# Kernel optimization log

Hardware: AMD Instinct MI355X
Metric: run time of the kernel (lower is better)

The kernel has to match this reference:

```python
import jax, jax.numpy as jnp
import numpy as np

B, S, H, F, E = 2, 2048, 1024, 4096, 8  # batch, seq, hidden, ffn, num_experts


def setup_inputs() -> dict:
    key = jax.random.key(0)
    ks = jax.random.split(key, 4)
    x = jax.random.normal(ks[0], (B, S, H), dtype=jnp.float32)
    w_router = jax.random.normal(ks[1], (H, E), dtype=jnp.float32) * 0.02
    w1 = jax.random.normal(ks[2], (E, H, F), dtype=jnp.float32) * 0.02
    b1 = jnp.zeros((E, F), dtype=jnp.float32)
    w2 = jax.random.normal(ks[3], (E, F, H), dtype=jnp.float32) * 0.02
    b2 = jnp.zeros((E, H), dtype=jnp.float32)
    return {"x": x, "w_router": w_router, "w1": w1, "b1": b1, "w2": w2, "b2": b2}


def reference(x, w_router, w1, b1, w2, b2):
    """Top-1 MoE layer: route -> per-expert FFN -> weighted combine.

    Faithful to ExpertParallelWrapper._process_moe_layer on a single group:
    router picks one expert per token with a routing weight; tokens are
    dispatched to experts (here expressed as a static mask over the fixed
    expert set), processed by the expert FFN, and scatter-combined back
    weighted by the routing probability.
    """
    Bs, Ss, Hs = x.shape
    n_experts = w1.shape[0]
    # Router: per-token logits -> softmax -> top-1 expert + weight
    logits = jnp.einsum('bsh,he->bse', x, w_router)          # [B,S,E]
    probs = jax.nn.softmax(logits, axis=-1)
    sel = jnp.argmax(probs, axis=-1)                          # [B,S] selected expert
    wgt = jnp.take_along_axis(probs, sel[..., None], axis=-1)[..., 0]  # [B,S]

    xt = x.reshape(-1, Hs)        # [T,H] flat tokens
    sel_t = sel.reshape(-1)       # [T]
    wgt_t = wgt.reshape(-1)       # [T]

    out = jnp.zeros_like(xt)
    # Static loop over the small fixed expert set (dispatch/combine via mask).
    for e in range(n_experts):
        h = jax.nn.relu(xt @ w1[e] + b1[e])   # [T,F]
        y = h @ w2[e] + b2[e]                 # [T,H]
        m = (sel_t == e).astype(xt.dtype) * wgt_t
        out = out + m[:, None] * y
    return out.reshape(Bs, Ss, Hs)
```

## Files before the change

kernel.cpp:

```cpp
#include <hip/hip_runtime.h>
#include <math.h>

#define T_TOK 4096
#define H_DIM 1024
#define F_DIM 4096
#define E_NUM 8
#define BK 32

typedef __attribute__((ext_vector_type(8))) short bhalf8_t;
typedef __attribute__((ext_vector_type(4))) float f32x4_t;

__device__ __forceinline__ unsigned short f2bf(float f) {
  unsigned int u = __float_as_uint(f);
  return (unsigned short)((u + 0x7fffu + ((u >> 16) & 1u)) >> 16);
}

__device__ __forceinline__ void gload16(const void* g, void* l) {
  __builtin_amdgcn_global_load_lds(
      (const __attribute__((address_space(1))) unsigned int*)g,
      (__attribute__((address_space(3))) unsigned int*)l, 16, 0, 0);
}

__global__ void k_init(int* counts) {
  if (threadIdx.x < E_NUM) counts[threadIdx.x] = 0;
}

__global__ void k_router(const float* __restrict__ x, const float* __restrict__ wr,
                         int* __restrict__ sel, float* __restrict__ wgt,
                         int* __restrict__ counts) {
  const int t = blockIdx.x;
  const int lane = threadIdx.x;
  const float* xr = x + (size_t)t * H_DIM;
  double acc[E_NUM] = {0, 0, 0, 0, 0, 0, 0, 0};
  for (int h = lane; h < H_DIM; h += 64) {
    const double xv = (double)xr[h];
    const float* w = wr + (size_t)h * E_NUM;
#pragma unroll
    for (int e = 0; e < E_NUM; ++e) acc[e] += xv * (double)w[e];
  }
#pragma unroll
  for (int e = 0; e < E_NUM; ++e) {
#pragma unroll
    for (int off = 32; off > 0; off >>= 1) acc[e] += __shfl_down(acc[e], off, 64);
  }
  if (lane == 0) {
    double m = acc[0];
    int a = 0;
#pragma unroll
    for (int e = 1; e < E_NUM; ++e)
      if (acc[e] > m) { m = acc[e]; a = e; }
    double s = 0.0;
#pragma unroll
    for (int e = 0; e < E_NUM; ++e) s += exp(acc[e] - m);
    sel[t] = a;
    wgt[t] = (float)(1.0 / s);
    atomicAdd(&counts[a], 1);
  }
}

__global__ void k_prefix(const int* __restrict__ counts, int* __restrict__ offs,
                         int* __restrict__ cursors) {
  if (threadIdx.x == 0 && blockIdx.x == 0) {
    int s = 0;
    for (int e = 0; e < E_NUM; ++e) {
      offs[e] = s;
      cursors[e] = s;
      s += counts[e];
    }
    offs[E_NUM] = s;
  }
}

__global__ void k_scatter(const float* __restrict__ x, const int* __restrict__ sel,
                          const float* __restrict__ wgt, int* __restrict__ cursors,
                          int* __restrict__ s2t, float* __restrict__ wgtS,
                          unsigned short* __restrict__ Xs) {
  const int t = blockIdx.x;
  __shared__ int sslot;
  if (threadIdx.x == 0) {
    const int slot = atomicAdd(&cursors[sel[t]], 1);
    sslot = slot;
    s2t[slot] = t;
    wgtS[slot] = wgt[t];
  }
  __syncthreads();
  const int slot = sslot;
  const float4 v = reinterpret_cast<const float4*>(x + (size_t)t * H_DIM)[threadIdx.x];
  ushort4 o;
  o.x = f2bf(v.x); o.y = f2bf(v.y); o.z = f2bf(v.z); o.w = f2bf(v.w);
  reinterpret_cast<ushort4*>(Xs + (size_t)slot * H_DIM)[threadIdx.x] = o;
}

__global__ void k_transpose(const float* __restrict__ in, unsigned short* __restrict__ out,
                            int K, int N) {
  const int e = blockIdx.z;
  const int n0 = blockIdx.x * 64;
  const int k0 = blockIdx.y * 64;
  __shared__ float tile[64][65];
  const float* src = in + (size_t)e * K * N;
  unsigned short* dst = out + (size_t)e * N * K;
  const int tx = threadIdx.x & 63;
  const int ty = threadIdx.x >> 6;
#pragma unroll
  for (int i = 0; i < 64; i += 4)
    tile[ty + i][tx] = src[(size_t)(k0 + ty + i) * N + (n0 + tx)];
  __syncthreads();
#pragma unroll
  for (int i = 0; i < 64; i += 4)
    dst[(size_t)(n0 + ty + i) * K + (k0 + tx)] = f2bf(tile[tx][ty + i]);
}

__global__ __launch_bounds__(256) void k_ffn1(const unsigned short* __restrict__ Xs,
                                              const unsigned short* __restrict__ Wt,
                                              const float* __restrict__ b1,
                                              unsigned short* __restrict__ Hws,
                                              const int* __restrict__ offs) {
  const int e = blockIdx.z;
  const int off = offs[e];
  const int cnt = offs[e + 1] - off;
  const int m0 = blockIdx.y * 128;
  if (m0 >= cnt) return;
  const int n0 = blockIdx.x * 128;
  const int msize = cnt - m0;

  __shared__ short lA[128 * BK];
  __shared__ short lB[128 * BK];

  const int tid = threadIdx.x;
  const int lane = tid & 63;
  const int wv = tid >> 6;
  const int wm = (wv >> 1) * 64;
  const int wn = (wv & 1) * 64;

  const int sRow = lane >> 2;
  const int sCol = (lane & 3) * 8;

  const unsigned short* Abase = Xs + (size_t)off * H_DIM;
  const unsigned short* Bbase = Wt + (size_t)e * F_DIM * H_DIM + (size_t)n0 * H_DIM;

  f32x4_t acc[4][4];
#pragma unroll
  for (int i = 0; i < 4; ++i)
#pragma unroll
    for (int j = 0; j < 4; ++j) acc[i][j] = (f32x4_t){0.f, 0.f, 0.f, 0.f};

  for (int k0 = 0; k0 < H_DIM; k0 += BK) {
    __syncthreads();
#pragma unroll
    for (int i = 0; i < 2; ++i) {
      const int g = wv * 2 + i;
      const int row = g * 16 + sRow;
      int ar = row;
      if (ar >= msize) ar = 0;
      gload16(Abase + (size_t)(m0 + ar) * H_DIM + k0 + sCol, &lA[g * 16 * BK]);
      gload16(Bbase + (size_t)row * H_DIM + k0 + sCol, &lB[g * 16 * BK]);
    }
    __syncthreads();

    const int q = lane >> 4;
    const int r16 = lane & 15;
    bhalf8_t af[4], bf[4];
#pragma unroll
    for (int mi = 0; mi < 4; ++mi)
      af[mi] = *reinterpret_cast<const bhalf8_t*>(&lA[(wm + mi * 16 + r16) * BK + q * 8]);
#pragma unroll
    for (int ni = 0; ni < 4; ++ni)
      bf[ni] = *reinterpret_cast<const bhalf8_t*>(&lB[(wn + ni * 16 + r16) * BK + q * 8]);
#pragma unroll
    for (int mi = 0; mi < 4; ++mi)
#pragma unroll
      for (int ni = 0; ni < 4; ++ni)
        acc[mi][ni] = __builtin_amdgcn_mfma_f32_16x16x32_bf16(af[mi], bf[ni], acc[mi][ni], 0, 0, 0);
  }

  const int q = lane >> 4;
  const int c = lane & 15;
#pragma unroll
  for (int ni = 0; ni < 4; ++ni) {
    const int col = n0 + wn + ni * 16 + c;
    const float bias = b1[e * F_DIM + col];
#pragma unroll
    for (int mi = 0; mi < 4; ++mi) {
      const int rbase = wm + mi * 16 + q * 4;
#pragma unroll
      for (int r = 0; r < 4; ++r) {
        const int row = rbase + r;
        if (row < msize) {
          float v = acc[mi][ni][r] + bias;
          v = fmaxf(v, 0.0f);
          Hws[(size_t)(off + m0 + row) * F_DIM + col] = f2bf(v);
        }
      }
    }
  }
}

__global__ __launch_bounds__(256) void k_ffn2(const unsigned short* __restrict__ Hws,
                                              const unsigned short* __restrict__ Wt,
                                              const float* __restrict__ b2,
                                              const int* __restrict__ offs,
                                              const int* __restrict__ s2t,
                                              const float* __restrict__ wgtS,
                                              float* __restrict__ out) {
  const int e = blockIdx.z;
  const int off = offs[e];
  const int cnt = offs[e + 1] - off;
  const int m0 = blockIdx.y * 128;
  if (m0 >= cnt) return;
  const int n0 = blockIdx.x * 128;
  const int msize = cnt - m0;

  __shared__ short lA[128 * BK];
  __shared__ short lB[128 * BK];

  const int tid = threadIdx.x;
  const int lane = tid & 63;
  const int wv = tid >> 6;
  const int wm = (wv >> 1) * 64;
  const int wn = (wv & 1) * 64;

  const int sRow = lane >> 2;
  const int sCol = (lane & 3) * 8;

  const unsigned short* Abase = Hws + (size_t)off * F_DIM;
  const unsigned short* Bbase = Wt + (size_t)e * H_DIM * F_DIM + (size_t)n0 * F_DIM;

  f32x4_t acc[4][4];
#pragma unroll
  for (int i = 0; i < 4; ++i)
#pragma unroll
    for (int j = 0; j < 4; ++j) acc[i][j] = (f32x4_t){0.f, 0.f, 0.f, 0.f};

  for (int k0 = 0; k0 < F_DIM; k0 += BK) {
    __syncthreads();
#pragma unroll
    for (int i = 0; i < 2; ++i) {
      const int g = wv * 2 + i;
      const int row = g * 16 + sRow;
      int ar = row;
      if (ar >= msize) ar = 0;
      gload16(Abase + (size_t)(m0 + ar) * F_DIM + k0 + sCol, &lA[g * 16 * BK]);
      gload16(Bbase + (size_t)row * F_DIM + k0 + sCol, &lB[g * 16 * BK]);
    }
    __syncthreads();

    const int q = lane >> 4;
    const int r16 = lane & 15;
    bhalf8_t af[4], bf[4];
#pragma unroll
    for (int mi = 0; mi < 4; ++mi)
      af[mi] = *reinterpret_cast<const bhalf8_t*>(&lA[(wm + mi * 16 + r16) * BK + q * 8]);
#pragma unroll
    for (int ni = 0; ni < 4; ++ni)
      bf[ni] = *reinterpret_cast<const bhalf8_t*>(&lB[(wn + ni * 16 + r16) * BK + q * 8]);
#pragma unroll
    for (int mi = 0; mi < 4; ++mi)
#pragma unroll
      for (int ni = 0; ni < 4; ++ni)
        acc[mi][ni] = __builtin_amdgcn_mfma_f32_16x16x32_bf16(af[mi], bf[ni], acc[mi][ni], 0, 0, 0);
  }

  const int q = lane >> 4;
  const int c = lane & 15;
#pragma unroll
  for (int mi = 0; mi < 4; ++mi) {
    const int rbase = wm + mi * 16 + q * 4;
#pragma unroll
    for (int r = 0; r < 4; ++r) {
      const int row = rbase + r;
      if (row >= msize) continue;
      const int srow = off + m0 + row;
      const int tok = s2t[srow];
      const float w = wgtS[srow];
      float* orow = out + (size_t)tok * H_DIM;
#pragma unroll
      for (int ni = 0; ni < 4; ++ni) {
        const int col = n0 + wn + ni * 16 + c;
        orow[col] = w * (acc[mi][ni][r] + b2[e * H_DIM + col]);
      }
    }
  }
}

extern "C" void kernel_launch(void* const* d_in, const int* in_sizes, int n_in,
                              void* d_out, int out_size, void* d_ws, size_t ws_size,
                              hipStream_t stream) {
  const float* x  = (const float*)d_in[0];
  const float* wr = (const float*)d_in[1];
  const float* w1 = (const float*)d_in[2];
  const float* b1 = (const float*)d_in[3];
  const float* w2 = (const float*)d_in[4];
  const float* b2 = (const float*)d_in[5];
  float* out = (float*)d_out;

  char* ws = (char*)d_ws;
  unsigned short* WT  = (unsigned short*)(ws);
  unsigned short* XS  = (unsigned short*)(ws + 67108864);
  unsigned short* HWS = (unsigned short*)(ws + 67108864 + 8388608);
  char* ctrl = ws + 67108864 + 8388608 + 33554432;
  int*   sel     = (int*)(ctrl);
  int*   s2t     = (int*)(ctrl + 16384);
  float* wgt     = (float*)(ctrl + 32768);
  float* wgtS    = (float*)(ctrl + 49152);
  int*   counts  = (int*)(ctrl + 65536);
  int*   offs    = (int*)(ctrl + 65536 + 64);
  int*   cursors = (int*)(ctrl + 65536 + 128);

  k_init<<<1, 64, 0, stream>>>(counts);
  k_router<<<T_TOK, 64, 0, stream>>>(x, wr, sel, wgt, counts);
  k_prefix<<<1, 1, 0, stream>>>(counts, offs, cursors);
  k_scatter<<<T_TOK, 256, 0, stream>>>(x, sel, wgt, cursors, s2t, wgtS, XS);

  k_transpose<<<dim3(F_DIM / 64, H_DIM / 64, E_NUM), 256, 0, stream>>>(w1, WT, H_DIM, F_DIM);
  k_ffn1<<<dim3(F_DIM / 128, T_TOK / 128, E_NUM), 256, 0, stream>>>(XS, WT, b1, HWS, offs);

  k_transpose<<<dim3(H_DIM / 64, F_DIM / 64, E_NUM), 256, 0, stream>>>(w2, WT, F_DIM, H_DIM);
  k_ffn2<<<dim3(H_DIM / 128, T_TOK / 128, E_NUM), 256, 0, stream>>>(HWS, WT, b2, offs, s2t, wgtS, out);
}
```

Measured before the change: 581.4 us.

## Double GEMM K-tile, XOR-swizzle LDS, vectorize transpose, pack router blocks

The expert GEMM K-tile grows from 32 to 64, halving the number of barrier-separated load/compute iterations, and the LDS layout gets an XOR swizzle on both the global-to-LDS loads and the fragment reads to avoid bank conflicts. The weight transpose kernel now uses float4 loads and 16-byte packed bf16 stores instead of scalar accesses. The router packs four tokens per 256-thread block, and the GEMMs get a launch-bounds occupancy hint. Costs are doubled LDS per block and possible register pressure from the hint.

```diff
diff --git a/kernel.cpp b/kernel.cpp
--- a/kernel.cpp
+++ b/kernel.cpp
@@ -5,9 +5,10 @@
 #define H_DIM 1024
 #define F_DIM 4096
 #define E_NUM 8
-#define BK 32
+#define BK 64
 
 typedef __attribute__((ext_vector_type(8))) short bhalf8_t;
+typedef __attribute__((ext_vector_type(8))) unsigned short ushort8_t;
 typedef __attribute__((ext_vector_type(4))) float f32x4_t;
 
 __device__ __forceinline__ unsigned short f2bf(float f) {
@@ -25,11 +26,12 @@
   if (threadIdx.x < E_NUM) counts[threadIdx.x] = 0;
 }
 
-__global__ void k_router(const float* __restrict__ x, const float* __restrict__ wr,
-                         int* __restrict__ sel, float* __restrict__ wgt,
-                         int* __restrict__ counts) {
-  const int t = blockIdx.x;
-  const int lane = threadIdx.x;
+__global__ __launch_bounds__(256) void k_router(const float* __restrict__ x,
+                                                const float* __restrict__ wr,
+                                                int* __restrict__ sel, float* __restrict__ wgt,
+                                                int* __restrict__ counts) {
+  const int t = blockIdx.x * 4 + (threadIdx.x >> 6);
+  const int lane = threadIdx.x & 63;
   const float* xr = x + (size_t)t * H_DIM;
   double acc[E_NUM] = {0, 0, 0, 0, 0, 0, 0, 0};
   for (int h = lane; h < H_DIM; h += 64) {
@@ -91,30 +93,44 @@
   reinterpret_cast<ushort4*>(Xs + (size_t)slot * H_DIM)[threadIdx.x] = o;
 }
 
-__global__ void k_transpose(const float* __restrict__ in, unsigned short* __restrict__ out,
-                            int K, int N) {
+__global__ __launch_bounds__(256) void k_transpose(const float* __restrict__ in,
+                                                   unsigned short* __restrict__ out,
+                                                   int K, int N) {
   const int e = blockIdx.z;
   const int n0 = blockIdx.x * 64;
   const int k0 = blockIdx.y * 64;
   __shared__ float tile[64][65];
   const float* src = in + (size_t)e * K * N;
   unsigned short* dst = out + (size_t)e * N * K;
-  const int tx = threadIdx.x & 63;
-  const int ty = threadIdx.x >> 6;
-#pragma unroll
-  for (int i = 0; i < 64; i += 4)
-    tile[ty + i][tx] = src[(size_t)(k0 + ty + i) * N + (n0 + tx)];
+  const int l = threadIdx.x;
+  const int lr = l >> 4;
+  const int lc = (l & 15) * 4;
+#pragma unroll
+  for (int i = 0; i < 64; i += 16) {
+    const float4 v = *reinterpret_cast<const float4*>(&src[(size_t)(k0 + lr + i) * N + n0 + lc]);
+    tile[lr + i][lc] = v.x;
+    tile[lr + i][lc + 1] = v.y;
+    tile[lr + i][lc + 2] = v.z;
+    tile[lr + i][lc + 3] = v.w;
+  }
   __syncthreads();
-#pragma unroll
-  for (int i = 0; i < 64; i += 4)
-    dst[(size_t)(n0 + ty + i) * K + (k0 + tx)] = f2bf(tile[tx][ty + i]);
-}
-
-__global__ __launch_bounds__(256) void k_ffn1(const unsigned short* __restrict__ Xs,
-                                              const unsigned short* __restrict__ Wt,
-                                              const float* __restrict__ b1,
-                                              unsigned short* __restrict__ Hws,
-                                              const int* __restrict__ offs) {
+  const int kk = (l & 7) * 8;
+  const int nr = l >> 3;
+#pragma unroll
+  for (int i = 0; i < 64; i += 32) {
+    const int n = nr + i;
+    ushort8_t o;
+#pragma unroll
+    for (int j = 0; j < 8; ++j) o[j] = f2bf(tile[kk + j][n]);
+    *reinterpret_cast<ushort8_t*>(&dst[(size_t)(n0 + n) * K + k0 + kk]) = o;
+  }
+}
+
+__global__ __launch_bounds__(256, 4) void k_ffn1(const unsigned short* __restrict__ Xs,
+                                                 const unsigned short* __restrict__ Wt,
+                                                 const float* __restrict__ b1,
+                                                 unsigned short* __restrict__ Hws,
+                                                 const int* __restrict__ offs) {
   const int e = blockIdx.z;
   const int off = offs[e];
   const int cnt = offs[e + 1] - off;
@@ -132,8 +148,9 @@
   const int wm = (wv >> 1) * 64;
   const int wn = (wv & 1) * 64;
 
-  const int sRow = lane >> 2;
-  const int sCol = (lane & 3) * 8;
+  const int sRow = lane >> 3;
+  const int cc = lane & 7;
+  const int gch = cc ^ sRow;
 
   const unsigned short* Abase = Xs + (size_t)off * H_DIM;
   const unsigned short* Bbase = Wt + (size_t)e * F_DIM * H_DIM + (size_t)n0 * H_DIM;
@@ -144,36 +161,40 @@
 #pragma unroll
     for (int j = 0; j < 4; ++j) acc[i][j] = (f32x4_t){0.f, 0.f, 0.f, 0.f};
 
+  const int q = lane >> 4;
+  const int r16 = lane & 15;
+  const int sw = r16 & 7;
+
   for (int k0 = 0; k0 < H_DIM; k0 += BK) {
     __syncthreads();
 #pragma unroll
-    for (int i = 0; i < 2; ++i) {
-      const int g = wv * 2 + i;
-      const int row = g * 16 + sRow;
-      int ar = row;
-      if (ar >= msize) ar = 0;
-      gload16(Abase + (size_t)(m0 + ar) * H_DIM + k0 + sCol, &lA[g * 16 * BK]);
-      gload16(Bbase + (size_t)row * H_DIM + k0 + sCol, &lB[g * 16 * BK]);
+    for (int i = 0; i < 4; ++i) {
+      const int g = wv * 4 + i;
+      const int row = g * 8 + sRow;
+      const int ar = (row < msize) ? row : 0;
+      gload16(Abase + (size_t)(m0 + ar) * H_DIM + k0 + gch * 8, &lA[g * 8 * BK]);
+      gload16(Bbase + (size_t)row * H_DIM + k0 + gch * 8, &lB[g * 8 * BK]);
     }
     __syncthreads();
 
-    const int q = lane >> 4;
-    const int r16 = lane & 15;
-    bhalf8_t af[4], bf[4];
-#pragma unroll
-    for (int mi = 0; mi < 4; ++mi)
-      af[mi] = *reinterpret_cast<const bhalf8_t*>(&lA[(wm + mi * 16 + r16) * BK + q * 8]);
-#pragma unroll
-    for (int ni = 0; ni < 4; ++ni)
-      bf[ni] = *reinterpret_cast<const bhalf8_t*>(&lB[(wn + ni * 16 + r16) * BK + q * 8]);
-#pragma unroll
-    for (int mi = 0; mi < 4; ++mi)
+#pragma unroll
+    for (int step = 0; step < 2; ++step) {
+      const int slot = (step * 4 + q) ^ sw;
+      bhalf8_t af[4], bf[4];
+#pragma unroll
+      for (int mi = 0; mi < 4; ++mi)
+        af[mi] = *reinterpret_cast<const bhalf8_t*>(&lA[(wm + mi * 16 + r16) * BK + slot * 8]);
 #pragma unroll
       for (int ni = 0; ni < 4; ++ni)
-        acc[mi][ni] = __builtin_amdgcn_mfma_f32_16x16x32_bf16(af[mi], bf[ni], acc[mi][ni], 0, 0, 0);
-  }
-
-  const int q = lane >> 4;
+        bf[ni] = *reinterpret_cast<const bhalf8_t*>(&lB[(wn + ni * 16 + r16) * BK + slot * 8]);
+#pragma unroll
+      for (int mi = 0; mi < 4; ++mi)
+#pragma unroll
+        for (int ni = 0; ni < 4; ++ni)
+          acc[mi][ni] = __builtin_amdgcn_mfma_f32_16x16x32_bf16(af[mi], bf[ni], acc[mi][ni], 0, 0, 0);
+    }
+  }
+
   const int c = lane & 15;
 #pragma unroll
   for (int ni = 0; ni < 4; ++ni) {
@@ -195,13 +216,13 @@
   }
 }
 
-__global__ __launch_bounds__(256) void k_ffn2(const unsigned short* __restrict__ Hws,
-                                              const unsigned short* __restrict__ Wt,
-                                              const float* __restrict__ b2,
-                                              const int* __restrict__ offs,
-                                              const int* __restrict__ s2t,
-                                              const float* __restrict__ wgtS,
-                                              float* __restrict__ out) {
+__global__ __launch_bounds__(256, 4) void k_ffn2(const unsigned short* __restrict__ Hws,
+                                                 const unsigned short* __restrict__ Wt,
+                                                 const float* __restrict__ b2,
+                                                 const int* __restrict__ offs,
+                                                 const int* __restrict__ s2t,
+                                                 const float* __restrict__ wgtS,
+                                                 float* __restrict__ out) {
   const int e = blockIdx.z;
   const int off = offs[e];
   const int cnt = offs[e + 1] - off;
@@ -219,8 +240,9 @@
   const int wm = (wv >> 1) * 64;
   const int wn = (wv & 1) * 64;
 
-  const int sRow = lane >> 2;
-  const int sCol = (lane & 3) * 8;
+  const int sRow = lane >> 3;
+  const int cc = lane & 7;
+  const int gch = cc ^ sRow;
 
   const unsigned short* Abase = Hws + (size_t)off * F_DIM;
   const unsigned short* Bbase = Wt + (size_t)e * H_DIM * F_DIM + (size_t)n0 * F_DIM;
@@ -231,36 +253,40 @@
 #pragma unroll
     for (int j = 0; j < 4; ++j) acc[i][j] = (f32x4_t){0.f, 0.f, 0.f, 0.f};
 
+  const int q = lane >> 4;
+  const int r16 = lane & 15;
+  const int sw = r16 & 7;
+
   for (int k0 = 0; k0 < F_DIM; k0 += BK) {
     __syncthreads();
 #pragma unroll
-    for (int i = 0; i < 2; ++i) {
-      const int g = wv * 2 + i;
-      const int row = g * 16 + sRow;
-      int ar = row;
-      if (ar >= msize) ar = 0;
-      gload16(Abase + (size_t)(m0 + ar) * F_DIM + k0 + sCol, &lA[g * 16 * BK]);
-      gload16(Bbase + (size_t)row * F_DIM + k0 + sCol, &lB[g * 16 * BK]);
+    for (int i = 0; i < 4; ++i) {
+      const int g = wv * 4 + i;
+      const int row = g * 8 + sRow;
+      const int ar = (row < msize) ? row : 0;
+      gload16(Abase + (size_t)(m0 + ar) * F_DIM + k0 + gch * 8, &lA[g * 8 * BK]);
+      gload16(Bbase + (size_t)row * F_DIM + k0 + gch * 8, &lB[g * 8 * BK]);
     }
     __syncthreads();
 
-    const int q = lane >> 4;
-    const int r16 = lane & 15;
-    bhalf8_t af[4], bf[4];
-#pragma unroll
-    for (int mi = 0; mi < 4; ++mi)
-      af[mi] = *reinterpret_cast<const bhalf8_t*>(&lA[(wm + mi * 16 + r16) * BK + q * 8]);
-#pragma unroll
-    for (int ni = 0; ni < 4; ++ni)
-      bf[ni] = *reinterpret_cast<const bhalf8_t*>(&lB[(wn + ni * 16 + r16) * BK + q * 8]);
-#pragma unroll
-    for (int mi = 0; mi < 4; ++mi)
+#pragma unroll
+    for (int step = 0; step < 2; ++step) {
+      const int slot = (step * 4 + q) ^ sw;
+      bhalf8_t af[4], bf[4];
+#pragma unroll
+      for (int mi = 0; mi < 4; ++mi)
+        af[mi] = *reinterpret_cast<const bhalf8_t*>(&lA[(wm + mi * 16 + r16) * BK + slot * 8]);
 #pragma unroll
       for (int ni = 0; ni < 4; ++ni)
-        acc[mi][ni] = __builtin_amdgcn_mfma_f32_16x16x32_bf16(af[mi], bf[ni], acc[mi][ni], 0, 0, 0);
-  }
-
-  const int q = lane >> 4;
+        bf[ni] = *reinterpret_cast<const bhalf8_t*>(&lB[(wn + ni * 16 + r16) * BK + slot * 8]);
+#pragma unroll
+      for (int mi = 0; mi < 4; ++mi)
+#pragma unroll
+        for (int ni = 0; ni < 4; ++ni)
+          acc[mi][ni] = __builtin_amdgcn_mfma_f32_16x16x32_bf16(af[mi], bf[ni], acc[mi][ni], 0, 0, 0);
+    }
+  }
+
   const int c = lane & 15;
 #pragma unroll
   for (int mi = 0; mi < 4; ++mi) {
@@ -307,7 +333,7 @@
   int*   cursors = (int*)(ctrl + 65536 + 128);
 
   k_init<<<1, 64, 0, stream>>>(counts);
-  k_router<<<T_TOK, 64, 0, stream>>>(x, wr, sel, wgt, counts);
+  k_router<<<T_TOK / 4, 256, 0, stream>>>(x, wr, sel, wgt, counts);
   k_prefix<<<1, 1, 0, stream>>>(counts, offs, cursors);
   k_scatter<<<T_TOK, 256, 0, stream>>>(x, sel, wgt, cursors, s2t, wgtS, XS);
 
```

Measured after the change: 579.9 us. No clear change (-0.3%).
